# Performance work log

Measured on AMD Instinct MI355X. Metric: run time of the kernel, lower is better.

The kernel has to match this reference:

```python
import jax, jax.numpy as jnp
import numpy as np

L, M, DCUT, HL = 8, 8, 6, 2   # lattice rows, cols, bond dim, local Hilbert dim
N = L * M                     # nqubits
B = 32768                     # batch of spin configurations


def setup_inputs() -> dict:
    key = jax.random.key(0)
    ks = jax.random.split(key, 8)
    s = 0.1
    return {
        "parm_M_h": jax.random.normal(ks[0], (L, M, HL, DCUT, DCUT), jnp.float32) * s,
        "parm_M_v": jax.random.normal(ks[1], (L, M, HL, DCUT, DCUT), jnp.float32) * s,
        "parm_v":   jax.random.normal(ks[2], (L, M, HL, DCUT), jnp.float32) * s,
        "parm_T":   jax.random.normal(ks[3], (L, M, HL, DCUT, DCUT, DCUT), jnp.float32) * s,
        "parm_w":   jax.random.normal(ks[4], (L, M, DCUT), jnp.float32) * s,
        "parm_c":   jnp.zeros((L, M), jnp.float32),
        "parm_eta": jax.random.normal(ks[5], (L, M, DCUT), jnp.float32),
        "x":        jax.random.randint(ks[6], (B, N), 0, 2, jnp.int32),  # occupation bits 0/1
    }


def _snake_ij():
    # snake traversal: row i left->right if i even, right->left if i odd
    i = np.repeat(np.arange(L), M)
    jm = np.tile(np.arange(M), L)
    j = np.where(i % 2 == 0, jm, M - 1 - jm)
    return i, j


def _forward(parm_M_h, parm_M_v, parm_v, parm_T, parm_w, parm_c, parm_eta, x):
    target = x.T.astype(jnp.int32)               # (N, B) bits, qubit k visited at scan step k
    ii, jj = _snake_ij()
    # gather per-site params in snake scan order -> leading axis N
    Mh = parm_M_h[ii, jj]; Mv = parm_M_v[ii, jj]; V = parm_v[ii, jj]
    T = parm_T[ii, jj];    W = parm_w[ii, jj];    C = parm_c[ii, jj]
    Eta = parm_eta[ii, jj]
    jcol = jnp.asarray(jj, jnp.int32)            # column index per step (vertical state slot)
    row_start = jnp.asarray(np.arange(N) % M == 0)

    def step(carry, xs):
        h_h, v_state, amp, phi = carry
        Mh_k, Mv_k, V_k, T_k, W_k, C_k, eta_k, t_k, j_k, rs = xs
        # left boundary (ones) at the start of each row
        h_h = jnp.where(rs, 1.0, h_h)                                  # (dcut, B)
        h_v = jax.lax.dynamic_index_in_dim(v_state, j_k, 0, keepdims=False)  # (dcut, B)
        # update_h: residual small einsums ('abc,bd->acd' in torch)
        hh2 = h_h[None] + jnp.einsum('aoc,cb->aob', Mh_k, h_h)          # (hl, dcut, B)
        hv2 = h_v[None] + jnp.einsum('aoc,cb->aob', Mv_k, h_v)
        tt = jnp.einsum('aocd,cb,db->aob', T_k, h_h, h_v)               # tensor term
        h_full = hh2 + hv2 + tt + V_k[:, :, None]
        # normalize hidden per sample for numerical stability
        h_full = h_full / jnp.sqrt(jnp.sum(h_full * h_full, axis=(0, 1), keepdims=True) + 1e-12)
        # conditional probabilities P(s) ~ sum_o eta_o^2 h[s,o]^2
        q = jnp.einsum('o,aob->ab', eta_k * eta_k, h_full * h_full)     # (hl, B)
        prob = q / jnp.sum(q, axis=0, keepdims=True)
        sel = (t_k == 1)
        p_sel = jnp.where(sel, prob[1], prob[0])
        h_sel = jnp.where(sel[None, :], h_full[1], h_full[0])           # (dcut, B)
        amp = amp * jnp.sqrt(p_sel)
        phi = phi + jnp.einsum('o,ob->b', W_k, h_sel) + C_k             # regular phase accumulation
        v_state = jax.lax.dynamic_update_index_in_dim(v_state, h_sel, j_k, 0)
        return (h_sel, v_state, amp, phi), None

    h0 = jnp.ones((DCUT, B), jnp.float32)
    v0 = jnp.zeros((M, DCUT, B), jnp.float32)   # bottom boundary: zeros
    amp0 = jnp.ones((B,), jnp.float32)
    phi0 = jnp.zeros((B,), jnp.float32)
    (_, _, amp, phi), _ = jax.lax.scan(
        step, (h0, v0, amp0, phi0),
        (Mh, Mv, V, T, W, C, Eta, target, jcol, row_start))
    return amp, phi


def reference(parm_M_h, parm_M_v, parm_v, parm_T, parm_w, parm_c, parm_eta, x):
    amp, phi = _forward(parm_M_h, parm_M_v, parm_v, parm_T, parm_w, parm_c, parm_eta, x)
    # psi = amp * exp(i*phi)
    return amp * jnp.cos(phi) + 1j * (amp * jnp.sin(phi))
```

## Files before the change

### kernel.cpp

```cpp
#include <hip/hip_runtime.h>
#include <hip/hip_fp16.h>
#include <math.h>


#define NQ  64
#define BT  256
#define SPB 64

typedef _Float16 h2v __attribute__((ext_vector_type(2)));
typedef __fp16  p2v __attribute__((ext_vector_type(2)));
union H2U { unsigned u; h2v h; __half2 hh; };

static __device__ __forceinline__ h2v pack2(float a, float b) {
    p2v p = __builtin_amdgcn_cvt_pkrtz(a, b);
    h2v r; __builtin_memcpy(&r, &p, sizeof(r));
    return r;
}
static __device__ __forceinline__ h2v u2h(unsigned u) {
    h2v r; __builtin_memcpy(&r, &u, sizeof(r));
    return r;
}
static __device__ __forceinline__ unsigned h2u(h2v h) {
    unsigned r; __builtin_memcpy(&r, &h, sizeof(r));
    return r;
}

#define DPPF(x, ctrl) __int_as_float(__builtin_amdgcn_update_dpp(            \
    __float_as_int(x), __float_as_int(x), (ctrl), 0xF, 0xF, false))
#define QP_XOR1 0xB1
#define QP_XOR2 0x4E
#define QP_BC0  0x00
#define QP_BC1  0x55

#if defined(__has_builtin)
#  if __has_builtin(__builtin_amdgcn_rcpf)
#    define FAST_RCP(x) __builtin_amdgcn_rcpf(x)
#  else
#    define FAST_RCP(x) (1.0f / (x))
#  endif
#  if __has_builtin(__builtin_amdgcn_rsqf)
#    define FAST_RSQ(x) __builtin_amdgcn_rsqf(x)
#  else
#    define FAST_RSQ(x) rsqrtf(x)
#  endif
#  if __has_builtin(__builtin_amdgcn_fdot2)
#    define HAS_FDOT2 1
#  endif
#else
#  define FAST_RCP(x) (1.0f / (x))
#  define FAST_RSQ(x) rsqrtf(x)
#endif

static __device__ __forceinline__ float fdot2u(unsigned a, h2v b, float c) {
#ifdef HAS_FDOT2
    H2U u; u.u = a;
    return __builtin_amdgcn_fdot2(u.h, b, c, false);
#else
    H2U u; u.u = a;
    return fmaf((float)u.h.x, (float)b.x, fmaf((float)u.h.y, (float)b.y, c));
#endif
}

__global__ __launch_bounds__(BT, 1) void mps_rnn16(
    const float* __restrict__ Mh,
    const float* __restrict__ Mv,
    const float* __restrict__ Vp,
    const float* __restrict__ Tp,
    const float* __restrict__ Wp,
    const float* __restrict__ Cp,
    const float* __restrict__ Ep,
    const int*   __restrict__ X,
    float*       __restrict__ out,
    int Bn, int writeImag)
{
    __shared__ unsigned Tl[16 * 12 * 24];
    __shared__ float    VE [16 * 4 * 8];
    __shared__ uint4    Wl [16];
    __shared__ unsigned vsm[8 * 64 * 4];

    const int t   = threadIdx.x;
    const int sub = t & 3;
    const int s   = t >> 2;
    int b = blockIdx.x * SPB + s;
    const bool valid = (b < Bn);
    if (!valid) b = Bn - 1;

    unsigned long long bits;
    {
        const int4* xr = reinterpret_cast<const int4*>(X + (size_t)b * NQ + sub * 16);
        unsigned long long part = 0ull;
        #pragma unroll
        for (int q = 0; q < 4; ++q) {
            int4 v = xr[q];
            part |= (unsigned long long)(v.x & 1) << (4 * q + 0);
            part |= (unsigned long long)(v.y & 1) << (4 * q + 1);
            part |= (unsigned long long)(v.z & 1) << (4 * q + 2);
            part |= (unsigned long long)(v.w & 1) << (4 * q + 3);
        }
        bits = part << (16 * sub);
        bits |= __shfl_xor(bits, 1, 64);
        bits |= __shfl_xor(bits, 2, 64);
    }

    for (int u = t; u < 8 * 64 * 4; u += BT) vsm[u] = 0u;

    const int mya = sub >> 1;
    const int ohi = sub & 1;
    (void)ohi;

    float hh[6];
    h2v hhp0, hhp1, hhp2;
    float amp2 = 1.f, phi = 0.f;

    for (int ch = 0; ch < 4; ++ch) {
        __syncthreads();
        {
            const float2* gT = reinterpret_cast<const float2*>(Tp + ch * 6912);
            for (int p = t; p < 3456; p += BT) {
                int site = p / 216, rr = p - site * 216;
                int row = rr / 18,  w  = rr - row * 18;
                float2 v = gT[p];
                H2U hu; hu.hh = __floats2half2_rn(v.x, v.y);
                Tl[(site * 12 + row) * 24 + w] = hu.u;
            }
            const float2* gH = reinterpret_cast<const float2*>(Mh + ch * 1152);
            const float2* gV = reinterpret_cast<const float2*>(Mv + ch * 1152);
            for (int p = t; p < 576; p += BT) {
                int site = p / 36, rr = p - site * 36;
                int row = rr / 3,  w  = rr - row * 3;
                int o_r = row - ((row >= 6) ? 6 : 0);
                float2 vh = gH[p], vv2 = gV[p];
                if ((o_r >> 1) == w) {
                    if (o_r & 1) { vh.y += 1.f; vv2.y += 1.f; }
                    else         { vh.x += 1.f; vv2.x += 1.f; }
                }
                H2U a; a.hh = __floats2half2_rn(vh.x, vh.y);
                H2U c; c.hh = __floats2half2_rn(vv2.x, vv2.y);
                Tl[(site * 12 + row) * 24 + 18 + w] = a.u;
                Tl[(site * 12 + row) * 24 + 21 + w] = c.u;
            }
            if (t < 192) {
                int site = t / 12, q = t - site * 12;
                int sb = q / 3,    c = q - sb * 3;
                VE[(site * 4 + sb) * 8 + c] = Vp[ch * 192 + t];
                float e = Ep[ch * 96 + site * 6 + (sb & 1) * 3 + c];
                VE[(site * 4 + sb) * 8 + 3 + c] = e * e;
            } else if (t < 208) {
                int site = t - 192;
                const float2* gw = reinterpret_cast<const float2*>(Wp) + ch * 48 + site * 3;
                float2 w01 = gw[0], w23 = gw[1], w45 = gw[2];
                H2U u0, u1, u2;
                u0.hh = __floats2half2_rn(w01.x, w01.y);
                u1.hh = __floats2half2_rn(w23.x, w23.y);
                u2.hh = __floats2half2_rn(w45.x, w45.y);
                Wl[site] = make_uint4(u0.u, u1.u, u2.u,
                                      __float_as_uint(Cp[ch * 16 + site]));
            }
        }
        __syncthreads();

        #pragma unroll
        for (int ih = 0; ih < 2; ++ih) {
            const unsigned cbr = (unsigned)(bits >> (ch * 16 + ih * 8)) & 0xFFu;

            #pragma unroll 2
            for (int qq = 0; qq < 8; ++qq) {
                const int j    = ih ? 7 - qq : qq;
                const int slot = ih * 8 + j;

                const unsigned* Tb = Tl + (slot * 12 + sub * 3) * 24;
                const float*   VEb = VE + (slot * 4 + sub) * 8;

                if (qq == 0) {
                    #pragma unroll
                    for (int o = 0; o < 6; ++o) hh[o] = 1.f;
                    H2U one; one.u = 0x3C003C00u;
                    hhp0 = one.h; hhp1 = one.h; hhp2 = one.h;
                }

                uint4 hvu = *reinterpret_cast<const uint4*>(vsm + j * 256 + s * 4);
                const h2v hvh0 = u2h(hvu.x);
                const h2v hvh1 = u2h(hvu.y);
                const h2v hvh2 = u2h(hvu.z);

                float4 ve0 = *reinterpret_cast<const float4*>(VEb);
                float2 ve1 = *reinterpret_cast<const float2*>(VEb + 4);
                const float vv_[3] = { ve0.x, ve0.y, ve0.z };
                const float e2_[3] = { ve0.w, ve1.x, ve1.y };

                float acc[3];
                #pragma unroll
                for (int lr = 0; lr < 3; ++lr) {
                    const unsigned* Tr = Tb + lr * 24;
                    uint4 tA = *reinterpret_cast<const uint4*>(Tr);
                    uint4 tB = *reinterpret_cast<const uint4*>(Tr + 4);
                    uint4 tC = *reinterpret_cast<const uint4*>(Tr + 8);
                    uint4 tD = *reinterpret_cast<const uint4*>(Tr + 12);
                    uint4 tE = *reinterpret_cast<const uint4*>(Tr + 16);
                    uint4 tF = *reinterpret_cast<const uint4*>(Tr + 20);
                    const unsigned tw[18] = {tA.x,tA.y,tA.z,tA.w, tB.x,tB.y,tB.z,tB.w,
                                             tC.x,tC.y,tC.z,tC.w, tD.x,tD.y,tD.z,tD.w,
                                             tE.x,tE.y};
                    float sc[6];
                    #pragma unroll
                    for (int c = 0; c < 6; ++c)
                        sc[c] = fdot2u(tw[c*3+0], hvh0,
                                fdot2u(tw[c*3+1], hvh1,
                                fdot2u(tw[c*3+2], hvh2, 0.f)));

                    float ta = fmaf(sc[0], hh[0], fmaf(sc[2], hh[2], sc[4]*hh[4]));
                    float tb = fmaf(sc[1], hh[1], fmaf(sc[3], hh[3], sc[5]*hh[5]));
                    float md = fdot2u(tE.z, hhp0, fdot2u(tE.w, hhp1,
                               fdot2u(tF.x, hhp2, vv_[lr])));
                    float nd = fdot2u(tF.y, hvh0, fdot2u(tF.z, hvh1,
                               fdot2u(tF.w, hvh2, 0.f)));
                    acc[lr] = (ta + tb) + (md + nd);
                }

                float q0_ = acc[0]*acc[0], q1_ = acc[1]*acc[1], q2_ = acc[2]*acc[2];
                float ssl = (q0_ + q1_) + q2_;
                float pq  = fmaf(e2_[0], q0_, fmaf(e2_[1], q1_, e2_[2] * q2_));
                float s1  = ssl + DPPF(ssl, QP_XOR1);
                float ssq = s1 + DPPF(s1, QP_XOR2);
                float p1  = pq + DPPF(pq, QP_XOR1);
                float px  = DPPF(p1, QP_XOR2);
                const float inv = FAST_RSQ(ssq + 1e-12f);

                const int sel = (cbr >> qq) & 1;
                const float qsel = (mya == sel) ? p1 : px;
                amp2 *= qsel * FAST_RCP(p1 + px);

                float an0 = acc[0] * inv, an1 = acc[1] * inv, an2 = acc[2] * inv;
                float sw0 = DPPF(an0, QP_XOR2);
                float sw1 = DPPF(an1, QP_XOR2);
                float sw2 = DPPF(an2, QP_XOR2);
                an0 = sel ? sw0 : an0;
                an1 = sel ? sw1 : an1;
                an2 = sel ? sw2 : an2;
                hh[0] = DPPF(an0, QP_BC0); hh[3] = DPPF(an0, QP_BC1);
                hh[1] = DPPF(an1, QP_BC0); hh[4] = DPPF(an1, QP_BC1);
                hh[2] = DPPF(an2, QP_BC0); hh[5] = DPPF(an2, QP_BC1);
                hhp0 = pack2(hh[0], hh[1]);
                hhp1 = pack2(hh[2], hh[3]);
                hhp2 = pack2(hh[4], hh[5]);

                uint4 wv = Wl[slot];
                phi = fdot2u(wv.x, hhp0, fdot2u(wv.y, hhp1,
                      fdot2u(wv.z, hhp2, __uint_as_float(wv.w) + phi)));

                if (sub == 0) {
                    *reinterpret_cast<uint4*>(vsm + j * 256 + s * 4) =
                        make_uint4(h2u(hhp0), h2u(hhp1), h2u(hhp2), 0u);
                }
            }
        }
    }

    if (sub == 0 && valid) {
        const float amp = sqrtf(amp2);
        if (writeImag) {
            out[2 * b + 0] = amp * cosf(phi);
            out[2 * b + 1] = amp * sinf(phi);
        } else {
            out[b] = amp * cosf(phi);
        }
    }
}

extern "C" void kernel_launch(void* const* d_in, const int* in_sizes, int n_in,
                              void* d_out, int out_size, void* d_ws, size_t ws_size,
                              hipStream_t stream) {
    const float* Mh = (const float*)d_in[0];
    const float* Mv = (const float*)d_in[1];
    const float* Vp = (const float*)d_in[2];
    const float* Tp = (const float*)d_in[3];
    const float* Wp = (const float*)d_in[4];
    const float* Cp = (const float*)d_in[5];
    const float* Ep = (const float*)d_in[6];
    const int*   X  = (const int*)d_in[7];
    float* out = (float*)d_out;

    const int Bn = in_sizes[7] / NQ;
    const int writeImag = (out_size >= 2 * Bn) ? 1 : 0;
    const int grid = (Bn + SPB - 1) / SPB;

    mps_rnn16<<<grid, BT, 0, stream>>>(Mh, Mv, Vp, Tp, Wp, Cp, Ep, X, out,
                                       Bn, writeImag);
}
```

Baseline: 65.03 us.

## Keep vertical MPS state in registers and shrink shared memory for higher occupancy

```diff
diff --git a/kernel.cpp b/kernel.cpp
--- a/kernel.cpp
+++ b/kernel.cpp
@@ -61,7 +61,7 @@
 #endif
 }
 
-__global__ __launch_bounds__(BT, 1) void mps_rnn16(
+__global__ __launch_bounds__(BT, 2) void mps_rnn17(
     const float* __restrict__ Mh,
     const float* __restrict__ Mv,
     const float* __restrict__ Vp,
@@ -74,14 +74,13 @@
     int Bn, int writeImag)
 {
     __shared__ unsigned Tl[16 * 12 * 24];
-    __shared__ float    VE [16 * 4 * 8];
-    __shared__ uint4    Wl [16];
-    __shared__ unsigned vsm[8 * 64 * 4];
+    __shared__ uint4    VEh[16 * 4];
 
     const int t   = threadIdx.x;
     const int sub = t & 3;
     const int s   = t >> 2;
-    int b = blockIdx.x * SPB + s;
+    (void)s;
+    int b = blockIdx.x * SPB + (t >> 2);
     const bool valid = (b < Bn);
     if (!valid) b = Bn - 1;
 
@@ -102,11 +101,11 @@
         bits |= __shfl_xor(bits, 2, 64);
     }
 
-    for (int u = t; u < 8 * 64 * 4; u += BT) vsm[u] = 0u;
-
     const int mya = sub >> 1;
-    const int ohi = sub & 1;
-    (void)ohi;
+
+    unsigned vsr0[8], vsr1[8], vsr2[8];
+    #pragma unroll
+    for (int j = 0; j < 8; ++j) { vsr0[j] = 0u; vsr1[j] = 0u; vsr2[j] = 0u; }
 
     float hh[6];
     h2v hhp0, hhp1, hhp2;
@@ -139,22 +138,16 @@
                 Tl[(site * 12 + row) * 24 + 18 + w] = a.u;
                 Tl[(site * 12 + row) * 24 + 21 + w] = c.u;
             }
-            if (t < 192) {
-                int site = t / 12, q = t - site * 12;
-                int sb = q / 3,    c = q - sb * 3;
-                VE[(site * 4 + sb) * 8 + c] = Vp[ch * 192 + t];
-                float e = Ep[ch * 96 + site * 6 + (sb & 1) * 3 + c];
-                VE[(site * 4 + sb) * 8 + 3 + c] = e * e;
-            } else if (t < 208) {
-                int site = t - 192;
-                const float2* gw = reinterpret_cast<const float2*>(Wp) + ch * 48 + site * 3;
-                float2 w01 = gw[0], w23 = gw[1], w45 = gw[2];
+            if (t < 64) {
+                int site = t >> 2, sb = t & 3;
+                const float* vp = Vp + ch * 192 + site * 12 + sb * 3;
+                const float* ep = Ep + ch * 96 + site * 6 + (sb & 1) * 3;
+                float e0 = ep[0], e1 = ep[1], e2v = ep[2];
                 H2U u0, u1, u2;
-                u0.hh = __floats2half2_rn(w01.x, w01.y);
-                u1.hh = __floats2half2_rn(w23.x, w23.y);
-                u2.hh = __floats2half2_rn(w45.x, w45.y);
-                Wl[site] = make_uint4(u0.u, u1.u, u2.u,
-                                      __float_as_uint(Cp[ch * 16 + site]));
+                u0.hh = __floats2half2_rn(vp[0], vp[1]);
+                u1.hh = __floats2half2_rn(vp[2], e0 * e0);
+                u2.hh = __floats2half2_rn(e1 * e1, e2v * e2v);
+                VEh[site * 4 + sb] = make_uint4(u0.u, u1.u, u2.u, 0u);
             }
         }
         __syncthreads();
@@ -163,13 +156,15 @@
         for (int ih = 0; ih < 2; ++ih) {
             const unsigned cbr = (unsigned)(bits >> (ch * 16 + ih * 8)) & 0xFFu;
 
-            #pragma unroll 2
+            #pragma unroll
             for (int qq = 0; qq < 8; ++qq) {
                 const int j    = ih ? 7 - qq : qq;
                 const int slot = ih * 8 + j;
+                const int siteg = ch * 16 + slot;
 
                 const unsigned* Tb = Tl + (slot * 12 + sub * 3) * 24;
-                const float*   VEb = VE + (slot * 4 + sub) * 8;
+                const float* wq = Wp + siteg * 6;
+                const float  ck = Cp[siteg];
 
                 if (qq == 0) {
                     #pragma unroll
@@ -178,15 +173,17 @@
                     hhp0 = one.h; hhp1 = one.h; hhp2 = one.h;
                 }
 
-                uint4 hvu = *reinterpret_cast<const uint4*>(vsm + j * 256 + s * 4);
-                const h2v hvh0 = u2h(hvu.x);
-                const h2v hvh1 = u2h(hvu.y);
-                const h2v hvh2 = u2h(hvu.z);
-
-                float4 ve0 = *reinterpret_cast<const float4*>(VEb);
-                float2 ve1 = *reinterpret_cast<const float2*>(VEb + 4);
-                const float vv_[3] = { ve0.x, ve0.y, ve0.z };
-                const float e2_[3] = { ve0.w, ve1.x, ve1.y };
+                const h2v hvh0 = u2h(vsr0[j]);
+                const h2v hvh1 = u2h(vsr1[j]);
+                const h2v hvh2 = u2h(vsr2[j]);
+
+                uint4 ve = VEh[slot * 4 + sub];
+                H2U e0u, e1u, e2u;
+                e0u.u = ve.x; e1u.u = ve.y; e2u.u = ve.z;
+                const float vv_[3] = { __low2float(e0u.hh), __high2float(e0u.hh),
+                                       __low2float(e1u.hh) };
+                const float e2_[3] = { __high2float(e1u.hh), __low2float(e2u.hh),
+                                       __high2float(e2u.hh) };
 
                 float acc[3];
                 #pragma unroll
@@ -244,14 +241,14 @@
                 hhp1 = pack2(hh[2], hh[3]);
                 hhp2 = pack2(hh[4], hh[5]);
 
-                uint4 wv = Wl[slot];
-                phi = fdot2u(wv.x, hhp0, fdot2u(wv.y, hhp1,
-                      fdot2u(wv.z, hhp2, __uint_as_float(wv.w) + phi)));
-
-                if (sub == 0) {
-                    *reinterpret_cast<uint4*>(vsm + j * 256 + s * 4) =
-                        make_uint4(h2u(hhp0), h2u(hhp1), h2u(hhp2), 0u);
-                }
+                float pA = fmaf(wq[1], hh[1], wq[0] * hh[0]);
+                float pB = fmaf(wq[3], hh[3], wq[2] * hh[2]);
+                float pC = fmaf(wq[5], hh[5], fmaf(wq[4], hh[4], ck));
+                phi += (pA + pB) + pC;
+
+                vsr0[j] = h2u(hhp0);
+                vsr1[j] = h2u(hhp1);
+                vsr2[j] = h2u(hhp2);
             }
         }
     }
@@ -284,6 +281,6 @@
     const int writeImag = (out_size >= 2 * Bn) ? 1 : 0;
     const int grid = (Bn + SPB - 1) / SPB;
 
-    mps_rnn16<<<grid, BT, 0, stream>>>(Mh, Mv, Vp, Tp, Wp, Cp, Ep, X, out,
+    mps_rnn17<<<grid, BT, 0, stream>>>(Mh, Mv, Vp, Tp, Wp, Cp, Ep, X, out,
                                        Bn, writeImag);
 }
```

Result: no change. 65.35 us (+0.5%).

## Prepack parameters in a separate kernel and forward vertical state in registers

Applied to the files above, without the earlier changes.

```diff
diff --git a/kernel.cpp b/kernel.cpp
--- a/kernel.cpp
+++ b/kernel.cpp
@@ -6,6 +6,7 @@
 #define NQ  64
 #define BT  256
 #define SPB 64
+#define CHUNK_U 5184
 
 typedef _Float16 h2v __attribute__((ext_vector_type(2)));
 typedef __fp16  p2v __attribute__((ext_vector_type(2)));
@@ -61,22 +62,72 @@
 #endif
 }
 
-__global__ __launch_bounds__(BT, 1) void mps_rnn16(
-    const float* __restrict__ Mh,
-    const float* __restrict__ Mv,
-    const float* __restrict__ Vp,
-    const float* __restrict__ Tp,
-    const float* __restrict__ Wp,
-    const float* __restrict__ Cp,
-    const float* __restrict__ Ep,
-    const int*   __restrict__ X,
-    float*       __restrict__ out,
-    int Bn, int writeImag)
+__global__ void repack_k(
+    const float* __restrict__ Mh, const float* __restrict__ Mv,
+    const float* __restrict__ Vp, const float* __restrict__ Tp,
+    const float* __restrict__ Wp, const float* __restrict__ Cp,
+    const float* __restrict__ Ep, unsigned* __restrict__ ws)
 {
-    __shared__ unsigned Tl[16 * 12 * 24];
-    __shared__ float    VE [16 * 4 * 8];
-    __shared__ uint4    Wl [16];
+    const int ch = blockIdx.x;
+    const int t  = threadIdx.x;
+    unsigned* Tm = ws + ch * CHUNK_U;
+    float*    VE = reinterpret_cast<float*>(Tm + 4608);
+    uint4*    Wl = reinterpret_cast<uint4*>(Tm + 4608 + 512);
+
+    const float2* gT = reinterpret_cast<const float2*>(Tp + ch * 6912);
+    for (int p = t; p < 3456; p += BT) {
+        int site = p / 216, rr = p - site * 216;
+        int row = rr / 18,  w  = rr - row * 18;
+        float2 v = gT[p];
+        H2U hu; hu.hh = __floats2half2_rn(v.x, v.y);
+        Tm[(site * 12 + row) * 24 + w] = hu.u;
+    }
+    const float2* gH = reinterpret_cast<const float2*>(Mh + ch * 1152);
+    const float2* gV = reinterpret_cast<const float2*>(Mv + ch * 1152);
+    for (int p = t; p < 576; p += BT) {
+        int site = p / 36, rr = p - site * 36;
+        int row = rr / 3,  w  = rr - row * 3;
+        int o_r = row - ((row >= 6) ? 6 : 0);
+        float2 vh = gH[p], vv2 = gV[p];
+        if ((o_r >> 1) == w) {
+            if (o_r & 1) { vh.y += 1.f; vv2.y += 1.f; }
+            else         { vh.x += 1.f; vv2.x += 1.f; }
+        }
+        H2U a; a.hh = __floats2half2_rn(vh.x, vh.y);
+        H2U c; c.hh = __floats2half2_rn(vv2.x, vv2.y);
+        Tm[(site * 12 + row) * 24 + 18 + w] = a.u;
+        Tm[(site * 12 + row) * 24 + 21 + w] = c.u;
+    }
+    if (t < 192) {
+        int site = t / 12, q = t - site * 12;
+        int sb = q / 3,    c = q - sb * 3;
+        VE[(site * 4 + sb) * 8 + c] = Vp[ch * 192 + t];
+        float e = Ep[ch * 96 + site * 6 + (sb & 1) * 3 + c];
+        VE[(site * 4 + sb) * 8 + 3 + c] = e * e;
+    } else if (t < 208) {
+        int site = t - 192;
+        const float2* gw = reinterpret_cast<const float2*>(Wp) + ch * 48 + site * 3;
+        float2 w01 = gw[0], w23 = gw[1], w45 = gw[2];
+        H2U u0, u1, u2;
+        u0.hh = __floats2half2_rn(w01.x, w01.y);
+        u1.hh = __floats2half2_rn(w23.x, w23.y);
+        u2.hh = __floats2half2_rn(w45.x, w45.y);
+        Wl[site] = make_uint4(u0.u, u1.u, u2.u,
+                              __float_as_uint(Cp[ch * 16 + site]));
+    }
+}
+
+__global__ __launch_bounds__(BT, 1) void mps_rnn20(
+    const unsigned* __restrict__ ws,
+    const int* __restrict__ X,
+    float* __restrict__ out, int Bn, int writeImag)
+{
+    __shared__ uint4    ldsb[CHUNK_U / 4];
     __shared__ unsigned vsm[8 * 64 * 4];
+
+    unsigned*     Tl = reinterpret_cast<unsigned*>(ldsb);
+    const float*  VE = reinterpret_cast<const float*>(Tl + 4608);
+    const uint4*  Wl = reinterpret_cast<const uint4*>(Tl + 4608 + 512);
 
     const int t   = threadIdx.x;
     const int sub = t & 3;
@@ -105,9 +156,173 @@
     for (int u = t; u < 8 * 64 * 4; u += BT) vsm[u] = 0u;
 
     const int mya = sub >> 1;
-    const int ohi = sub & 1;
-    (void)ohi;
-
+
+    float hh[6];
+    h2v hhp0, hhp1, hhp2;
+    float amp2 = 1.f, phi = 0.f;
+
+    for (int ch = 0; ch < 4; ++ch) {
+        __syncthreads();
+        {
+            const uint4* g4 = reinterpret_cast<const uint4*>(ws + ch * CHUNK_U);
+            #pragma unroll
+            for (int i = 0; i < 6; ++i) {
+                int idx = t + i * BT;
+                if (idx < CHUNK_U / 4) ldsb[idx] = g4[idx];
+            }
+        }
+        __syncthreads();
+
+        #pragma unroll
+        for (int ih = 0; ih < 2; ++ih) {
+            const unsigned cbr = (unsigned)(bits >> (ch * 16 + ih * 8)) & 0xFFu;
+
+            #pragma unroll 2
+            for (int qq = 0; qq < 8; ++qq) {
+                const int j    = ih ? 7 - qq : qq;
+                const int slot = ih * 8 + j;
+
+                const unsigned* Tb = Tl + (slot * 12 + sub * 3) * 24;
+                const float*   VEb = VE + (slot * 4 + sub) * 8;
+
+                h2v hvh0, hvh1, hvh2;
+                if (qq == 0) {
+                    if (ch == 0 && ih == 0) {
+                        H2U z; z.u = 0u;
+                        hvh0 = z.h; hvh1 = z.h; hvh2 = z.h;
+                    } else {
+                        hvh0 = hhp0; hvh1 = hhp1; hvh2 = hhp2;
+                    }
+                    #pragma unroll
+                    for (int o = 0; o < 6; ++o) hh[o] = 1.f;
+                    H2U one; one.u = 0x3C003C00u;
+                    hhp0 = one.h; hhp1 = one.h; hhp2 = one.h;
+                } else {
+                    uint4 hvu = *reinterpret_cast<const uint4*>(vsm + j * 256 + s * 4);
+                    hvh0 = u2h(hvu.x); hvh1 = u2h(hvu.y); hvh2 = u2h(hvu.z);
+                }
+
+                float4 ve0 = *reinterpret_cast<const float4*>(VEb);
+                float2 ve1 = *reinterpret_cast<const float2*>(VEb + 4);
+                const float vv_[3] = { ve0.x, ve0.y, ve0.z };
+                const float e2_[3] = { ve0.w, ve1.x, ve1.y };
+
+                float acc[3];
+                #pragma unroll
+                for (int lr = 0; lr < 3; ++lr) {
+                    const unsigned* Tr = Tb + lr * 24;
+                    uint4 tA = *reinterpret_cast<const uint4*>(Tr);
+                    uint4 tB = *reinterpret_cast<const uint4*>(Tr + 4);
+                    uint4 tC = *reinterpret_cast<const uint4*>(Tr + 8);
+                    uint4 tD = *reinterpret_cast<const uint4*>(Tr + 12);
+                    uint4 tE = *reinterpret_cast<const uint4*>(Tr + 16);
+                    uint4 tF = *reinterpret_cast<const uint4*>(Tr + 20);
+                    const unsigned tw[18] = {tA.x,tA.y,tA.z,tA.w, tB.x,tB.y,tB.z,tB.w,
+                                             tC.x,tC.y,tC.z,tC.w, tD.x,tD.y,tD.z,tD.w,
+                                             tE.x,tE.y};
+                    float sc[6];
+                    #pragma unroll
+                    for (int c = 0; c < 6; ++c)
+                        sc[c] = fdot2u(tw[c*3+0], hvh0,
+                                fdot2u(tw[c*3+1], hvh1,
+                                fdot2u(tw[c*3+2], hvh2, 0.f)));
+
+                    float ta = fmaf(sc[0], hh[0], fmaf(sc[2], hh[2], sc[4]*hh[4]));
+                    float tb = fmaf(sc[1], hh[1], fmaf(sc[3], hh[3], sc[5]*hh[5]));
+                    float md = fdot2u(tE.z, hhp0, fdot2u(tE.w, hhp1,
+                               fdot2u(tF.x, hhp2, vv_[lr])));
+                    float nd = fdot2u(tF.y, hvh0, fdot2u(tF.z, hvh1,
+                               fdot2u(tF.w, hvh2, 0.f)));
+                    acc[lr] = (ta + tb) + (md + nd);
+                }
+
+                float q0_ = acc[0]*acc[0], q1_ = acc[1]*acc[1], q2_ = acc[2]*acc[2];
+                float ssl = (q0_ + q1_) + q2_;
+                float pq  = fmaf(e2_[0], q0_, fmaf(e2_[1], q1_, e2_[2] * q2_));
+                float s1  = ssl + DPPF(ssl, QP_XOR1);
+                float ssq = s1 + DPPF(s1, QP_XOR2);
+                float p1  = pq + DPPF(pq, QP_XOR1);
+                float px  = DPPF(p1, QP_XOR2);
+                const float inv = FAST_RSQ(ssq + 1e-12f);
+
+                const int sel = (cbr >> qq) & 1;
+                const float qsel = (mya == sel) ? p1 : px;
+                amp2 *= qsel * FAST_RCP(p1 + px);
+
+                float an0 = acc[0] * inv, an1 = acc[1] * inv, an2 = acc[2] * inv;
+                float sw0 = DPPF(an0, QP_XOR2);
+                float sw1 = DPPF(an1, QP_XOR2);
+                float sw2 = DPPF(an2, QP_XOR2);
+                an0 = sel ? sw0 : an0;
+                an1 = sel ? sw1 : an1;
+                an2 = sel ? sw2 : an2;
+                hh[0] = DPPF(an0, QP_BC0); hh[3] = DPPF(an0, QP_BC1);
+                hh[1] = DPPF(an1, QP_BC0); hh[4] = DPPF(an1, QP_BC1);
+                hh[2] = DPPF(an2, QP_BC0); hh[5] = DPPF(an2, QP_BC1);
+                hhp0 = pack2(hh[0], hh[1]);
+                hhp1 = pack2(hh[2], hh[3]);
+                hhp2 = pack2(hh[4], hh[5]);
+
+                uint4 wv = Wl[slot];
+                phi = fdot2u(wv.x, hhp0, fdot2u(wv.y, hhp1,
+                      fdot2u(wv.z, hhp2, __uint_as_float(wv.w) + phi)));
+
+                if (sub == 0 && qq != 7) {
+                    *reinterpret_cast<uint4*>(vsm + j * 256 + s * 4) =
+                        make_uint4(h2u(hhp0), h2u(hhp1), h2u(hhp2), 0u);
+                }
+            }
+        }
+    }
+
+    if (sub == 0 && valid) {
+        const float amp = sqrtf(amp2);
+        if (writeImag) {
+            out[2 * b + 0] = amp * cosf(phi);
+            out[2 * b + 1] = amp * sinf(phi);
+        } else {
+            out[b] = amp * cosf(phi);
+        }
+    }
+}
+
+__global__ __launch_bounds__(BT, 1) void mps_rnn16fb(
+    const float* __restrict__ Mh, const float* __restrict__ Mv,
+    const float* __restrict__ Vp, const float* __restrict__ Tp,
+    const float* __restrict__ Wp, const float* __restrict__ Cp,
+    const float* __restrict__ Ep, const int* __restrict__ X,
+    float* __restrict__ out, int Bn, int writeImag)
+{
+    __shared__ unsigned Tl[16 * 12 * 24];
+    __shared__ float    VE [16 * 4 * 8];
+    __shared__ uint4    Wl [16];
+    __shared__ unsigned vsm[8 * 64 * 4];
+
+    const int t   = threadIdx.x;
+    const int sub = t & 3;
+    const int s   = t >> 2;
+    int b = blockIdx.x * SPB + s;
+    const bool valid = (b < Bn);
+    if (!valid) b = Bn - 1;
+
+    unsigned long long bits;
+    {
+        const int4* xr = reinterpret_cast<const int4*>(X + (size_t)b * NQ + sub * 16);
+        unsigned long long part = 0ull;
+        #pragma unroll
+        for (int q = 0; q < 4; ++q) {
+            int4 v = xr[q];
+            part |= (unsigned long long)(v.x & 1) << (4 * q + 0);
+            part |= (unsigned long long)(v.y & 1) << (4 * q + 1);
+            part |= (unsigned long long)(v.z & 1) << (4 * q + 2);
+            part |= (unsigned long long)(v.w & 1) << (4 * q + 3);
+        }
+        bits = part << (16 * sub);
+        bits |= __shfl_xor(bits, 1, 64);
+        bits |= __shfl_xor(bits, 2, 64);
+    }
+    for (int u = t; u < 8 * 64 * 4; u += BT) vsm[u] = 0u;
+    const int mya = sub >> 1;
     float hh[6];
     h2v hhp0, hhp1, hhp2;
     float amp2 = 1.f, phi = 0.f;
@@ -162,32 +377,26 @@
         #pragma unroll
         for (int ih = 0; ih < 2; ++ih) {
             const unsigned cbr = (unsigned)(bits >> (ch * 16 + ih * 8)) & 0xFFu;
-
             #pragma unroll 2
             for (int qq = 0; qq < 8; ++qq) {
                 const int j    = ih ? 7 - qq : qq;
                 const int slot = ih * 8 + j;
-
                 const unsigned* Tb = Tl + (slot * 12 + sub * 3) * 24;
                 const float*   VEb = VE + (slot * 4 + sub) * 8;
-
                 if (qq == 0) {
                     #pragma unroll
                     for (int o = 0; o < 6; ++o) hh[o] = 1.f;
                     H2U one; one.u = 0x3C003C00u;
                     hhp0 = one.h; hhp1 = one.h; hhp2 = one.h;
                 }
-
                 uint4 hvu = *reinterpret_cast<const uint4*>(vsm + j * 256 + s * 4);
                 const h2v hvh0 = u2h(hvu.x);
                 const h2v hvh1 = u2h(hvu.y);
                 const h2v hvh2 = u2h(hvu.z);
-
                 float4 ve0 = *reinterpret_cast<const float4*>(VEb);
                 float2 ve1 = *reinterpret_cast<const float2*>(VEb + 4);
                 const float vv_[3] = { ve0.x, ve0.y, ve0.z };
                 const float e2_[3] = { ve0.w, ve1.x, ve1.y };
-
                 float acc[3];
                 #pragma unroll
                 for (int lr = 0; lr < 3; ++lr) {
@@ -207,7 +416,6 @@
                         sc[c] = fdot2u(tw[c*3+0], hvh0,
                                 fdot2u(tw[c*3+1], hvh1,
                                 fdot2u(tw[c*3+2], hvh2, 0.f)));
-
                     float ta = fmaf(sc[0], hh[0], fmaf(sc[2], hh[2], sc[4]*hh[4]));
                     float tb = fmaf(sc[1], hh[1], fmaf(sc[3], hh[3], sc[5]*hh[5]));
                     float md = fdot2u(tE.z, hhp0, fdot2u(tE.w, hhp1,
@@ -216,7 +424,6 @@
                                fdot2u(tF.w, hvh2, 0.f)));
                     acc[lr] = (ta + tb) + (md + nd);
                 }
-
                 float q0_ = acc[0]*acc[0], q1_ = acc[1]*acc[1], q2_ = acc[2]*acc[2];
                 float ssl = (q0_ + q1_) + q2_;
                 float pq  = fmaf(e2_[0], q0_, fmaf(e2_[1], q1_, e2_[2] * q2_));
@@ -225,11 +432,9 @@
                 float p1  = pq + DPPF(pq, QP_XOR1);
                 float px  = DPPF(p1, QP_XOR2);
                 const float inv = FAST_RSQ(ssq + 1e-12f);
-
                 const int sel = (cbr >> qq) & 1;
                 const float qsel = (mya == sel) ? p1 : px;
                 amp2 *= qsel * FAST_RCP(p1 + px);
-
                 float an0 = acc[0] * inv, an1 = acc[1] * inv, an2 = acc[2] * inv;
                 float sw0 = DPPF(an0, QP_XOR2);
                 float sw1 = DPPF(an1, QP_XOR2);
@@ -243,11 +448,9 @@
                 hhp0 = pack2(hh[0], hh[1]);
                 hhp1 = pack2(hh[2], hh[3]);
                 hhp2 = pack2(hh[4], hh[5]);
-
                 uint4 wv = Wl[slot];
                 phi = fdot2u(wv.x, hhp0, fdot2u(wv.y, hhp1,
                       fdot2u(wv.z, hhp2, __uint_as_float(wv.w) + phi)));
-
                 if (sub == 0) {
                     *reinterpret_cast<uint4*>(vsm + j * 256 + s * 4) =
                         make_uint4(h2u(hhp0), h2u(hhp1), h2u(hhp2), 0u);
@@ -284,6 +487,14 @@
     const int writeImag = (out_size >= 2 * Bn) ? 1 : 0;
     const int grid = (Bn + SPB - 1) / SPB;
 
-    mps_rnn16<<<grid, BT, 0, stream>>>(Mh, Mv, Vp, Tp, Wp, Cp, Ep, X, out,
-                                       Bn, writeImag);
-}
+    const size_t need = (size_t)4 * CHUNK_U * sizeof(unsigned);
+    if (ws_size >= need) {
+        repack_k<<<4, BT, 0, stream>>>(Mh, Mv, Vp, Tp, Wp, Cp, Ep,
+                                       (unsigned*)d_ws);
+        mps_rnn20<<<grid, BT, 0, stream>>>((const unsigned*)d_ws, X, out,
+                                           Bn, writeImag);
+    } else {
+        mps_rnn16fb<<<grid, BT, 0, stream>>>(Mh, Mv, Vp, Tp, Wp, Cp, Ep, X,
+                                             out, Bn, writeImag);
+    }
+}
```

Result: faster. 63.33 us (-2.6%).

## Use one thread per sample with prepacked per-site params in workspace

Applied to the files above, without the earlier changes.

```diff
diff --git a/kernel.cpp b/kernel.cpp
--- a/kernel.cpp
+++ b/kernel.cpp
@@ -4,8 +4,9 @@
 
 
 #define NQ  64
-#define BT  256
-#define SPB 64
+#define BT  64
+#define SLOT_U 312
+#define WS_NEED (64 * SLOT_U * 4)
 
 typedef _Float16 h2v __attribute__((ext_vector_type(2)));
 typedef __fp16  p2v __attribute__((ext_vector_type(2)));
@@ -61,17 +62,180 @@
 #endif
 }
 
-__global__ __launch_bounds__(BT, 1) void mps_rnn16(
-    const float* __restrict__ Mh,
-    const float* __restrict__ Mv,
-    const float* __restrict__ Vp,
-    const float* __restrict__ Tp,
-    const float* __restrict__ Wp,
-    const float* __restrict__ Cp,
-    const float* __restrict__ Ep,
-    const int*   __restrict__ X,
-    float*       __restrict__ out,
-    int Bn, int writeImag)
+__global__ void repack23(
+    const float* __restrict__ Mh, const float* __restrict__ Mv,
+    const float* __restrict__ Vp, const float* __restrict__ Tp,
+    const float* __restrict__ Wp, const float* __restrict__ Cp,
+    const float* __restrict__ Ep, unsigned* __restrict__ ws)
+{
+    const int k = blockIdx.x;
+    const int t = threadIdx.x;
+    const int i = k >> 3, jm = k & 7;
+    const int j = (i & 1) ? 7 - jm : jm;
+    const int site = i * 8 + j;
+    unsigned* S = ws + k * SLOT_U;
+    float*    F = reinterpret_cast<float*>(S + 288);
+
+    const float2* gT = reinterpret_cast<const float2*>(Tp + site * 432);
+    for (int p = t; p < 216; p += BT) {
+        int row = p / 18, w = p - row * 18;
+        float2 v = gT[p];
+        H2U hu; hu.hh = __floats2half2_rn(v.x, v.y);
+        S[row * 24 + w] = hu.u;
+    }
+    const float2* gH = reinterpret_cast<const float2*>(Mh + site * 72);
+    const float2* gV = reinterpret_cast<const float2*>(Mv + site * 72);
+    if (t < 36) {
+        int row = t / 3, w = t - row * 3;
+        int o_r = row - ((row >= 6) ? 6 : 0);
+        float2 vh = gH[t], vv2 = gV[t];
+        if ((o_r >> 1) == w) {
+            if (o_r & 1) { vh.y += 1.f; vv2.y += 1.f; }
+            else         { vh.x += 1.f; vv2.x += 1.f; }
+        }
+        H2U a; a.hh = __floats2half2_rn(vh.x, vh.y);
+        H2U c; c.hh = __floats2half2_rn(vv2.x, vv2.y);
+        S[row * 24 + 18 + w] = a.u;
+        S[row * 24 + 21 + w] = c.u;
+    } else if (t < 48) {
+        F[t - 36] = Vp[site * 12 + (t - 36)];
+    } else if (t < 54) {
+        float e = Ep[site * 6 + (t - 48)];
+        F[12 + (t - 48)] = e * e;
+    } else if (t < 57) {
+        const float2* gw = reinterpret_cast<const float2*>(Wp + site * 6);
+        float2 wp = gw[t - 54];
+        H2U u; u.hh = __floats2half2_rn(wp.x, wp.y);
+        S[306 + (t - 54)] = u.u;
+    } else if (t == 57) {
+        F[21] = Cp[site];
+    }
+}
+
+__global__ __launch_bounds__(BT) void mps_rnn23(
+    const unsigned* __restrict__ ws,
+    const int* __restrict__ X,
+    float* __restrict__ out, int Bn, int writeImag)
+{
+    __shared__ unsigned v0[512], v1[512], v2[512];
+
+    const int lane = threadIdx.x;
+    int b = blockIdx.x * BT + lane;
+    const bool valid = (b < Bn);
+    if (!valid) b = Bn - 1;
+
+    unsigned long long bits = 0ull;
+    {
+        const int4* xr = reinterpret_cast<const int4*>(X + (size_t)b * NQ);
+        #pragma unroll
+        for (int q = 0; q < 16; ++q) {
+            int4 v = xr[q];
+            bits |= (unsigned long long)(v.x & 1) << (4 * q + 0);
+            bits |= (unsigned long long)(v.y & 1) << (4 * q + 1);
+            bits |= (unsigned long long)(v.z & 1) << (4 * q + 2);
+            bits |= (unsigned long long)(v.w & 1) << (4 * q + 3);
+        }
+    }
+
+    #pragma unroll
+    for (int jj = 0; jj < 8; ++jj) {
+        v0[jj * 64 + lane] = 0u;
+        v1[jj * 64 + lane] = 0u;
+        v2[jj * 64 + lane] = 0u;
+    }
+
+    float hh[6];
+    h2v hhp0, hhp1, hhp2;
+    float amp2 = 1.f, phi = 0.f;
+
+    #pragma unroll 2
+    for (int k = 0; k < NQ; ++k) {
+        const int jm  = k & 7;
+        const int dir = (k >> 3) & 1;
+        const int j   = dir ? 7 - jm : jm;
+        const unsigned* P = ws + k * SLOT_U;
+        const float*    F = reinterpret_cast<const float*>(P + 288);
+
+        if (jm == 0) {
+            #pragma unroll
+            for (int o = 0; o < 6; ++o) hh[o] = 1.f;
+            H2U one; one.u = 0x3C003C00u;
+            hhp0 = one.h; hhp1 = one.h; hhp2 = one.h;
+        }
+
+        const int vi = j * 64 + lane;
+        const h2v hv0 = u2h(v0[vi]);
+        const h2v hv1 = u2h(v1[vi]);
+        const h2v hv2 = u2h(v2[vi]);
+
+        float h[12];
+        #pragma unroll
+        for (int r = 0; r < 12; ++r) {
+            const unsigned* R = P + r * 24;
+            float sc0 = fdot2u(R[0],  hv0, fdot2u(R[1],  hv1, fdot2u(R[2],  hv2, 0.f)));
+            float sc1 = fdot2u(R[3],  hv0, fdot2u(R[4],  hv1, fdot2u(R[5],  hv2, 0.f)));
+            float sc2 = fdot2u(R[6],  hv0, fdot2u(R[7],  hv1, fdot2u(R[8],  hv2, 0.f)));
+            float sc3 = fdot2u(R[9],  hv0, fdot2u(R[10], hv1, fdot2u(R[11], hv2, 0.f)));
+            float sc4 = fdot2u(R[12], hv0, fdot2u(R[13], hv1, fdot2u(R[14], hv2, 0.f)));
+            float sc5 = fdot2u(R[15], hv0, fdot2u(R[16], hv1, fdot2u(R[17], hv2, 0.f)));
+            float ta = fmaf(sc0, hh[0], fmaf(sc2, hh[2], sc4 * hh[4]));
+            float tb = fmaf(sc1, hh[1], fmaf(sc3, hh[3], sc5 * hh[5]));
+            float md = fdot2u(R[18], hhp0, fdot2u(R[19], hhp1,
+                       fdot2u(R[20], hhp2, F[r])));
+            float nd = fdot2u(R[21], hv0, fdot2u(R[22], hv1,
+                       fdot2u(R[23], hv2, 0.f)));
+            h[r] = (ta + tb) + (md + nd);
+        }
+
+        float hsq[12];
+        #pragma unroll
+        for (int r = 0; r < 12; ++r) hsq[r] = h[r] * h[r];
+        float sA = (hsq[0] + hsq[1]) + (hsq[2] + hsq[3]);
+        float sB = (hsq[4] + hsq[5]) + (hsq[6] + hsq[7]);
+        float sC = (hsq[8] + hsq[9]) + (hsq[10] + hsq[11]);
+        const float ss = (sA + sB) + sC;
+        float q0 = fmaf(F[12], hsq[0], fmaf(F[13], hsq[1], fmaf(F[14], hsq[2],
+                   fmaf(F[15], hsq[3], fmaf(F[16], hsq[4], F[17] * hsq[5])))));
+        float q1 = fmaf(F[12], hsq[6], fmaf(F[13], hsq[7], fmaf(F[14], hsq[8],
+                   fmaf(F[15], hsq[9], fmaf(F[16], hsq[10], F[17] * hsq[11])))));
+        const float inv = FAST_RSQ(ss + 1e-12f);
+
+        const int sel = (int)((bits >> k) & 1ull);
+        const float psel = sel ? q1 : q0;
+        amp2 *= psel * FAST_RCP(q0 + q1);
+
+        #pragma unroll
+        for (int o = 0; o < 6; ++o)
+            hh[o] = (sel ? h[6 + o] : h[o]) * inv;
+        hhp0 = pack2(hh[0], hh[1]);
+        hhp1 = pack2(hh[2], hh[3]);
+        hhp2 = pack2(hh[4], hh[5]);
+
+        phi = fdot2u(P[306], hhp0, fdot2u(P[307], hhp1,
+              fdot2u(P[308], hhp2, F[21] + phi)));
+
+        v0[vi] = h2u(hhp0);
+        v1[vi] = h2u(hhp1);
+        v2[vi] = h2u(hhp2);
+    }
+
+    if (valid) {
+        const float amp = sqrtf(amp2);
+        if (writeImag) {
+            out[2 * b + 0] = amp * cosf(phi);
+            out[2 * b + 1] = amp * sinf(phi);
+        } else {
+            out[b] = amp * cosf(phi);
+        }
+    }
+}
+
+__global__ __launch_bounds__(256, 1) void mps_rnn16fb(
+    const float* __restrict__ Mh, const float* __restrict__ Mv,
+    const float* __restrict__ Vp, const float* __restrict__ Tp,
+    const float* __restrict__ Wp, const float* __restrict__ Cp,
+    const float* __restrict__ Ep, const int* __restrict__ X,
+    float* __restrict__ out, int Bn, int writeImag)
 {
     __shared__ unsigned Tl[16 * 12 * 24];
     __shared__ float    VE [16 * 4 * 8];
@@ -81,7 +245,7 @@
     const int t   = threadIdx.x;
     const int sub = t & 3;
     const int s   = t >> 2;
-    int b = blockIdx.x * SPB + s;
+    int b = blockIdx.x * 64 + s;
     const bool valid = (b < Bn);
     if (!valid) b = Bn - 1;
 
@@ -101,13 +265,8 @@
         bits |= __shfl_xor(bits, 1, 64);
         bits |= __shfl_xor(bits, 2, 64);
     }
-
-    for (int u = t; u < 8 * 64 * 4; u += BT) vsm[u] = 0u;
-
+    for (int u = t; u < 8 * 64 * 4; u += 256) vsm[u] = 0u;
     const int mya = sub >> 1;
-    const int ohi = sub & 1;
-    (void)ohi;
-
     float hh[6];
     h2v hhp0, hhp1, hhp2;
     float amp2 = 1.f, phi = 0.f;
@@ -116,7 +275,7 @@
         __syncthreads();
         {
             const float2* gT = reinterpret_cast<const float2*>(Tp + ch * 6912);
-            for (int p = t; p < 3456; p += BT) {
+            for (int p = t; p < 3456; p += 256) {
                 int site = p / 216, rr = p - site * 216;
                 int row = rr / 18,  w  = rr - row * 18;
                 float2 v = gT[p];
@@ -125,7 +284,7 @@
             }
             const float2* gH = reinterpret_cast<const float2*>(Mh + ch * 1152);
             const float2* gV = reinterpret_cast<const float2*>(Mv + ch * 1152);
-            for (int p = t; p < 576; p += BT) {
+            for (int p = t; p < 576; p += 256) {
                 int site = p / 36, rr = p - site * 36;
                 int row = rr / 3,  w  = rr - row * 3;
                 int o_r = row - ((row >= 6) ? 6 : 0);
@@ -162,32 +321,26 @@
         #pragma unroll
         for (int ih = 0; ih < 2; ++ih) {
             const unsigned cbr = (unsigned)(bits >> (ch * 16 + ih * 8)) & 0xFFu;
-
             #pragma unroll 2
             for (int qq = 0; qq < 8; ++qq) {
                 const int j    = ih ? 7 - qq : qq;
                 const int slot = ih * 8 + j;
-
                 const unsigned* Tb = Tl + (slot * 12 + sub * 3) * 24;
                 const float*   VEb = VE + (slot * 4 + sub) * 8;
-
                 if (qq == 0) {
                     #pragma unroll
                     for (int o = 0; o < 6; ++o) hh[o] = 1.f;
                     H2U one; one.u = 0x3C003C00u;
                     hhp0 = one.h; hhp1 = one.h; hhp2 = one.h;
                 }
-
                 uint4 hvu = *reinterpret_cast<const uint4*>(vsm + j * 256 + s * 4);
                 const h2v hvh0 = u2h(hvu.x);
                 const h2v hvh1 = u2h(hvu.y);
                 const h2v hvh2 = u2h(hvu.z);
-
                 float4 ve0 = *reinterpret_cast<const float4*>(VEb);
                 float2 ve1 = *reinterpret_cast<const float2*>(VEb + 4);
                 const float vv_[3] = { ve0.x, ve0.y, ve0.z };
                 const float e2_[3] = { ve0.w, ve1.x, ve1.y };
-
                 float acc[3];
                 #pragma unroll
                 for (int lr = 0; lr < 3; ++lr) {
@@ -207,7 +360,6 @@
                         sc[c] = fdot2u(tw[c*3+0], hvh0,
                                 fdot2u(tw[c*3+1], hvh1,
                                 fdot2u(tw[c*3+2], hvh2, 0.f)));
-
                     float ta = fmaf(sc[0], hh[0], fmaf(sc[2], hh[2], sc[4]*hh[4]));
                     float tb = fmaf(sc[1], hh[1], fmaf(sc[3], hh[3], sc[5]*hh[5]));
                     float md = fdot2u(tE.z, hhp0, fdot2u(tE.w, hhp1,
@@ -216,7 +368,6 @@
                                fdot2u(tF.w, hvh2, 0.f)));
                     acc[lr] = (ta + tb) + (md + nd);
                 }
-
                 float q0_ = acc[0]*acc[0], q1_ = acc[1]*acc[1], q2_ = acc[2]*acc[2];
                 float ssl = (q0_ + q1_) + q2_;
                 float pq  = fmaf(e2_[0], q0_, fmaf(e2_[1], q1_, e2_[2] * q2_));
@@ -225,11 +376,9 @@
                 float p1  = pq + DPPF(pq, QP_XOR1);
                 float px  = DPPF(p1, QP_XOR2);
                 const float inv = FAST_RSQ(ssq + 1e-12f);
-
                 const int sel = (cbr >> qq) & 1;
                 const float qsel = (mya == sel) ? p1 : px;
                 amp2 *= qsel * FAST_RCP(p1 + px);
-
                 float an0 = acc[0] * inv, an1 = acc[1] * inv, an2 = acc[2] * inv;
                 float sw0 = DPPF(an0, QP_XOR2);
                 float sw1 = DPPF(an1, QP_XOR2);
@@ -243,11 +392,9 @@
                 hhp0 = pack2(hh[0], hh[1]);
                 hhp1 = pack2(hh[2], hh[3]);
                 hhp2 = pack2(hh[4], hh[5]);
-
                 uint4 wv = Wl[slot];
                 phi = fdot2u(wv.x, hhp0, fdot2u(wv.y, hhp1,
                       fdot2u(wv.z, hhp2, __uint_as_float(wv.w) + phi)));
-
                 if (sub == 0) {
                     *reinterpret_cast<uint4*>(vsm + j * 256 + s * 4) =
                         make_uint4(h2u(hhp0), h2u(hhp1), h2u(hhp2), 0u);
@@ -282,8 +429,16 @@
 
     const int Bn = in_sizes[7] / NQ;
     const int writeImag = (out_size >= 2 * Bn) ? 1 : 0;
-    const int grid = (Bn + SPB - 1) / SPB;
-
-    mps_rnn16<<<grid, BT, 0, stream>>>(Mh, Mv, Vp, Tp, Wp, Cp, Ep, X, out,
-                                       Bn, writeImag);
-}
+
+    if (ws_size >= (size_t)WS_NEED) {
+        repack23<<<64, BT, 0, stream>>>(Mh, Mv, Vp, Tp, Wp, Cp, Ep,
+                                        (unsigned*)d_ws);
+        const int grid = (Bn + BT - 1) / BT;
+        mps_rnn23<<<grid, BT, 0, stream>>>((const unsigned*)d_ws, X, out,
+                                           Bn, writeImag);
+    } else {
+        const int grid = (Bn + 63) / 64;
+        mps_rnn16fb<<<grid, 256, 0, stream>>>(Mh, Mv, Vp, Tp, Wp, Cp, Ep, X,
+                                              out, Bn, writeImag);
+    }
+}
```

Result: slower. 229.4 us (+252.8%).
